# Kernel optimization log

Measured on AMD Instinct MI355X. Metric: run time of the kernel, lower is better.

## Reference

```python
import jax, jax.numpy as jnp
import numpy as np

EPS = 1e-6
N_HEADS = 6
N_POINTS = 4
B, LQ, C = 1, 96 * 96, 768


def _ln(x, w, b):
    mu = x.mean(-1, keepdims=True)
    var = ((x - mu) ** 2).mean(-1, keepdims=True)
    return (x - mu) * jax.lax.rsqrt(var + EPS) * w + b


def _corner(vbh, yi, xi, H, W):
    # vbh: [B, nH, H*W, Dh]; yi/xi: [B, nH, Lq, P] int32. Zero-padded OOB (grid_sample padding_mode='zeros').
    valid = (yi >= 0) & (yi < H) & (xi >= 0) & (xi < W)
    idx = jnp.clip(yi, 0, H - 1) * W + jnp.clip(xi, 0, W - 1)
    b, nh, lq, p = idx.shape
    g = jnp.take_along_axis(vbh, idx.reshape(b, nh, lq * p, 1), axis=2)
    g = g.reshape(b, nh, lq, p, vbh.shape[-1])
    return jnp.where(valid[..., None], g, jnp.zeros((), g.dtype))


def _msdeform(q, ref, feat, ss, so_w, so_b, aw_w, aw_b, vp_w, vp_b, op_w, op_b):
    # MSDeformAttn core: q [B,Lq,C], ref [B,Lq,L,2] in [0,1], feat [B,Len_in,C], ss np.int64 [L,2]=(H,W)
    b, lq, c = q.shape
    L = ss.shape[0]
    dh = c // N_HEADS
    value = (feat @ vp_w.T + vp_b).reshape(b, -1, N_HEADS, dh)
    offs = (q @ so_w.T + so_b).reshape(b, lq, N_HEADS, L, N_POINTS, 2)
    aw = jax.nn.softmax((q @ aw_w.T + aw_b).reshape(b, lq, N_HEADS, L * N_POINTS), -1)
    aw = aw.reshape(b, lq, N_HEADS, L, N_POINTS)
    # offset normalizer is (W, H) per level
    norm = jnp.asarray(np.ascontiguousarray(ss[:, ::-1]), dtype=q.dtype)  # [L,2]
    loc = ref[:, :, None, :, None, :] + offs / norm[None, None, None, :, None, :]
    out = jnp.zeros((b, N_HEADS, lq, dh), q.dtype)
    start = 0
    for l in range(L):
        H, W = int(ss[l, 0]), int(ss[l, 1])
        vbh = value[:, start:start + H * W].transpose(0, 2, 1, 3)  # [B,nH,H*W,Dh]
        # align_corners=False pixel coords: px = loc*W - 0.5
        px = loc[:, :, :, l, :, 0].transpose(0, 2, 1, 3) * W - 0.5  # [B,nH,Lq,P]
        py = loc[:, :, :, l, :, 1].transpose(0, 2, 1, 3) * H - 0.5
        x0 = jnp.floor(px).astype(jnp.int32)
        y0 = jnp.floor(py).astype(jnp.int32)
        fx = (px - x0)[..., None]
        fy = (py - y0)[..., None]
        samp = (_corner(vbh, y0, x0, H, W) * (1 - fy) * (1 - fx)
                + _corner(vbh, y0, x0 + 1, H, W) * (1 - fy) * fx
                + _corner(vbh, y0 + 1, x0, H, W) * fy * (1 - fx)
                + _corner(vbh, y0 + 1, x0 + 1, H, W) * fy * fx)  # [B,nH,Lq,P,Dh]
        w_l = aw[:, :, :, l, :].transpose(0, 2, 1, 3)[..., None]  # [B,nH,Lq,P,1]
        out = out + (samp * w_l).sum(3)
        start += H * W
    out = out.transpose(0, 2, 1, 3).reshape(b, lq, c)
    return out @ op_w.T + op_b


def setup_inputs() -> dict:
    key = jax.random.key(0)
    ks = jax.random.split(key, 14)
    lin = lambda k, o, i: 0.02 * jax.random.normal(k, (o, i), jnp.float32)
    return dict(
        query=jax.random.normal(ks[0], (B, LQ, C), jnp.float32),
        reference_points=jax.random.uniform(ks[1], (B, LQ, 1, 2), jnp.float32),
        feat=jax.random.normal(ks[2], (B, LQ, C), jnp.float32),
        feat_other_modalities=jax.random.normal(ks[3], (B, LQ, C), jnp.float32),
        spatial_shapes=np.array([[96, 96]], dtype=np.int64),
        level_start_index=np.array([0], dtype=np.int64),
        qn_w=jnp.ones(C), qn_b=jnp.zeros(C),
        fn_w=jnp.ones(C), fn_b=jnp.zeros(C),
        so_w=lin(ks[4], N_HEADS * N_POINTS * 2, C), so_b=0.02 * jax.random.normal(ks[12], (N_HEADS * N_POINTS * 2,), jnp.float32),
        aw_w=lin(ks[5], N_HEADS * N_POINTS, C), aw_b=jnp.zeros(N_HEADS * N_POINTS),
        vp_w=lin(ks[6], C, C), vp_b=jnp.zeros(C),
        op_w=lin(ks[7], C, C), op_b=jnp.zeros(C),
        gamma=0.02 * jax.random.normal(ks[8], (C,), jnp.float32),
        qn2_w=jnp.ones(C), qn2_b=jnp.zeros(C),
        fn2_w=jnp.ones(C), fn2_b=jnp.zeros(C),
        so2_w=lin(ks[9], N_HEADS * N_POINTS * 2, C), so2_b=0.02 * jax.random.normal(ks[13], (N_HEADS * N_POINTS * 2,), jnp.float32),
        aw2_w=lin(ks[10], N_HEADS * N_POINTS, C), aw2_b=jnp.zeros(N_HEADS * N_POINTS),
        vp2_w=lin(ks[11], C, C), vp2_b=jnp.zeros(C),
        op2_w=lin(jax.random.fold_in(key, 99), C, C), op2_b=jnp.zeros(C),
        gamma2=0.02 * jax.random.normal(jax.random.fold_in(key, 100), (C,), jnp.float32),
    )


def reference(query, reference_points, feat, feat_other_modalities, spatial_shapes, level_start_index,
              qn_w, qn_b, fn_w, fn_b, so_w, so_b, aw_w, aw_b, vp_w, vp_b, op_w, op_b, gamma,
              qn2_w, qn2_b, fn2_w, fn2_b, so2_w, so2_b, aw2_w, aw2_b, vp2_w, vp2_b, op2_w, op2_b, gamma2):
    ss = np.asarray(spatial_shapes)
    a = _msdeform(_ln(query, qn_w, qn_b), reference_points, _ln(feat, fn_w, fn_b), ss,
                  so_w, so_b, aw_w, aw_b, vp_w, vp_b, op_w, op_b)
    q = query + gamma * a
    a2 = _msdeform(_ln(q, qn2_w, qn2_b), reference_points,
                   _ln(feat_other_modalities, fn2_w, fn2_b), ss,
                   so2_w, so2_b, aw2_w, aw2_b, vp2_w, vp2_b, op2_w, op2_b)
    return q + gamma2 * a2
```

## Files before the change

kernel.cpp:

```cpp
#include <hip/hip_runtime.h>
#include <hip/hip_bf16.h>

typedef unsigned short u16;
typedef unsigned int u32;
typedef __attribute__((ext_vector_type(8))) short bf16x8;
typedef __attribute__((ext_vector_type(4))) float f32x4;
typedef __attribute__((ext_vector_type(4))) u32 u32x4;

#define LQ 9216
#define CC 768
#define NH 6
#define DH 128
#define HH 96
#define WW 96

__device__ __forceinline__ u16 f2bf(float f) {
  union { float f; u32 u; } x; x.f = f;
  u32 r = x.u + 0x7fff + ((x.u >> 16) & 1);
  return (u16)(r >> 16);
}
__device__ __forceinline__ float u2f(u32 u) {
  union { u32 u; float f; } x; x.u = u; return x.f;
}

__device__ __forceinline__ void gl_lds16(const void* g, void* l) {
  __builtin_amdgcn_global_load_lds((const __attribute__((address_space(1))) void*)g,
                                   (__attribute__((address_space(3))) void*)l, 16, 0, 0);
}

__global__ __launch_bounds__(256)
void prep_weights(const float* __restrict__ vp, const float* __restrict__ op,
                  const float* __restrict__ vp2, const float* __restrict__ op2,
                  const float* __restrict__ so, const float* __restrict__ aw,
                  const float* __restrict__ so2, const float* __restrict__ aw2,
                  const float* __restrict__ so_b, const float* __restrict__ aw_b,
                  const float* __restrict__ so2_b, const float* __restrict__ aw2_b,
                  u16* __restrict__ w4, u16* __restrict__ cat1, u16* __restrict__ cat2,
                  float* __restrict__ b1, float* __restrict__ b2) {
  const int i = blockIdx.x * 256 + threadIdx.x;
  const int NW = 589824;
  if (i < 4 * NW) {
    const int m = i / NW, r = i - m * NW;
    const float* s = (m == 0) ? vp : (m == 1) ? op : (m == 2) ? vp2 : op2;
    w4[i] = f2bf(s[r]);
  } else if (i < 4 * NW + 2 * 98304) {
    const int j = i - 4 * NW;
    const int which = j / 98304;
    const int r = j - which * 98304;
    const int row = r / 768, colr = r - row * 768;
    float v = 0.f;
    if (row < 48) v = (which ? so2 : so)[row * 768 + colr];
    else if (row < 72) v = (which ? aw2 : aw)[(row - 48) * 768 + colr];
    (which ? cat2 : cat1)[r] = f2bf(v);
  } else if (i < 4 * NW + 2 * 98304 + 256) {
    const int j = i - 4 * NW - 2 * 98304;
    const int which = j >> 7, row = j & 127;
    float v = 0.f;
    if (row < 48) v = (which ? so2_b : so_b)[row];
    else if (row < 72) v = (which ? aw2_b : aw_b)[row - 48];
    (which ? b2 : b1)[row] = v;
  }
}

__device__ __forceinline__ void ln_body(const float* __restrict__ x, const float* __restrict__ w,
                                        const float* __restrict__ b, u16* __restrict__ out, int row) {
  const int t = threadIdx.x;
  const float* xr = x + (size_t)row * CC;
  float v0 = xr[t], v1 = xr[t + 256], v2 = xr[t + 512];
  float s = v0 + v1 + v2;
  float ss = v0 * v0 + v1 * v1 + v2 * v2;
  #pragma unroll
  for (int o = 32; o > 0; o >>= 1) {
    s += __shfl_xor(s, o, 64);
    ss += __shfl_xor(ss, o, 64);
  }
  __shared__ float rs[4], rss[4];
  const int wv = t >> 6, ln = t & 63;
  if (ln == 0) { rs[wv] = s; rss[wv] = ss; }
  __syncthreads();
  s = rs[0] + rs[1] + rs[2] + rs[3];
  ss = rss[0] + rss[1] + rss[2] + rss[3];
  const float mu = s * (1.f / 768.f);
  const float var = ss * (1.f / 768.f) - mu * mu;
  const float rstd = rsqrtf(var + 1e-6f);
  u16* orow = out + (size_t)row * CC;
  orow[t]       = f2bf((v0 - mu) * rstd * w[t]       + b[t]);
  orow[t + 256] = f2bf((v1 - mu) * rstd * w[t + 256] + b[t + 256]);
  orow[t + 512] = f2bf((v2 - mu) * rstd * w[t + 512] + b[t + 512]);
}

__global__ __launch_bounds__(256)
void ln_to_bf16(const float* __restrict__ x, const float* __restrict__ w,
                const float* __restrict__ b, u16* __restrict__ out) {
  ln_body(x, w, b, out, blockIdx.x);
}

__global__ __launch_bounds__(256)
void ln3_to_bf16(const float* __restrict__ x0, const float* __restrict__ w0, const float* __restrict__ b0, u16* __restrict__ o0,
                 const float* __restrict__ x1, const float* __restrict__ w1, const float* __restrict__ b1, u16* __restrict__ o1,
                 const float* __restrict__ x2, const float* __restrict__ w2, const float* __restrict__ b2, u16* __restrict__ o2) {
  const int sel = blockIdx.y;
  const float* x = (sel == 0) ? x0 : (sel == 1) ? x1 : x2;
  const float* w = (sel == 0) ? w0 : (sel == 1) ? w1 : w2;
  const float* b = (sel == 0) ? b0 : (sel == 1) ? b1 : b2;
  u16* o = (sel == 0) ? o0 : (sel == 1) ? o1 : o2;
  ln_body(x, w, b, o, blockIdx.x);
}

template <int MODE>
__device__ __forceinline__ void gemm_core(const u16* __restrict__ A, const u16* __restrict__ W,
                                          const float* __restrict__ bias, void* __restrict__ outv,
                                          const float* __restrict__ res, const float* __restrict__ gamma,
                                          int M, int N, int K, int m0, int n0) {
  __shared__ u16 As[128 * 32];
  __shared__ u16 Bs[128 * 32];
  const int tid = threadIdx.x;
  const int wv = tid >> 6, lane = tid & 63;
  const int quad = lane >> 4, l16 = lane & 15;
  const int wm = wv & 1, wn = wv >> 1;
  const int srow = (wv << 4) + (lane >> 2);
  const int scol = (lane & 3) << 3;

  f32x4 acc[4][4];
  #pragma unroll
  for (int i = 0; i < 4; ++i)
    #pragma unroll
    for (int j = 0; j < 4; ++j)
      acc[i][j] = (f32x4){0.f, 0.f, 0.f, 0.f};

  const u16* ag = A + (size_t)(m0 + srow) * K + scol;
  const u16* bg = W + (size_t)(n0 + srow) * K + scol;
  u16* la = As + wv * 512 + lane * 8;
  u16* lb = Bs + wv * 512 + lane * 8;

  for (int k0 = 0; k0 < K; k0 += 32) {
    __syncthreads();
    gl_lds16(ag + k0, la);
    gl_lds16(ag + (size_t)64 * K + k0, la + 2048);
    gl_lds16(bg + k0, lb);
    gl_lds16(bg + (size_t)64 * K + k0, lb + 2048);
    __syncthreads();
    bf16x8 af[4], bfr[4];
    #pragma unroll
    for (int i = 0; i < 4; ++i)
      af[i] = *(const bf16x8*)(As + ((wm * 64 + i * 16 + l16) * 32 + quad * 8));
    #pragma unroll
    for (int j = 0; j < 4; ++j)
      bfr[j] = *(const bf16x8*)(Bs + ((wn * 64 + j * 16 + l16) * 32 + quad * 8));
    #pragma unroll
    for (int i = 0; i < 4; ++i)
      #pragma unroll
      for (int j = 0; j < 4; ++j)
        acc[i][j] = __builtin_amdgcn_mfma_f32_16x16x32_bf16(af[i], bfr[j], acc[i][j], 0, 0, 0);
  }

  #pragma unroll
  for (int i = 0; i < 4; ++i) {
    #pragma unroll
    for (int j = 0; j < 4; ++j) {
      const int col = n0 + wn * 64 + j * 16 + l16;
      const float bs = bias[col];
      #pragma unroll
      for (int r = 0; r < 4; ++r) {
        const int row = m0 + wm * 64 + i * 16 + quad * 4 + r;
        const float v = acc[i][j][r] + bs;
        const size_t o = (size_t)row * N + col;
        if (MODE == 0) ((u16*)outv)[o] = f2bf(v);
        else if (MODE == 1) ((float*)outv)[o] = v;
        else ((float*)outv)[o] = res[o] + gamma[col] * v;
      }
    }
  }
}

template <int MODE>
__global__ __launch_bounds__(256)
void gemm_bt(const u16* __restrict__ A, const u16* __restrict__ W,
             const float* __restrict__ bias, void* __restrict__ outv,
             const float* __restrict__ res, const float* __restrict__ gamma,
             int M, int N, int K) {
  gemm_core<MODE>(A, W, bias, outv, res, gamma, M, N, K, blockIdx.x * 128, blockIdx.y * 128);
}

__global__ __launch_bounds__(256)
void gemm_val_dual(const u16* __restrict__ A0, const u16* __restrict__ W0, const float* __restrict__ b0, u16* __restrict__ o0,
                   const u16* __restrict__ A1, const u16* __restrict__ W1, const float* __restrict__ b1, u16* __restrict__ o1,
                   int M, int N, int K) {
  const int z = blockIdx.z;
  const u16* A = z ? A1 : A0;
  const u16* W = z ? W1 : W0;
  const float* b = z ? b1 : b0;
  u16* o = z ? o1 : o0;
  gemm_core<0>(A, W, b, (void*)o, nullptr, nullptr, M, N, K, blockIdx.x * 128, blockIdx.y * 128);
}

__global__ __launch_bounds__(256)
void gemm_small(const u16* __restrict__ A, const u16* __restrict__ W,
                const float* __restrict__ bias, float* __restrict__ out,
                int M, int N, int K) {
  __shared__ u16 As[64 * 32];
  __shared__ u16 Bs[64 * 32];
  const int tid = threadIdx.x;
  const int wv = tid >> 6, lane = tid & 63;
  const int quad = lane >> 4, l16 = lane & 15;
  const int wm = wv & 1, wn = wv >> 1;
  const int m0 = blockIdx.x * 64, n0 = blockIdx.y * 64;
  const int srow = tid >> 2;
  const int scol = (tid & 3) << 3;

  f32x4 acc[2][2];
  #pragma unroll
  for (int i = 0; i < 2; ++i)
    #pragma unroll
    for (int j = 0; j < 2; ++j)
      acc[i][j] = (f32x4){0.f, 0.f, 0.f, 0.f};

  const u16* ag = A + (size_t)(m0 + srow) * K + scol;
  const u16* bg = W + (size_t)(n0 + srow) * K + scol;
  u16* la = As + tid * 8;
  u16* lb = Bs + tid * 8;

  for (int k0 = 0; k0 < K; k0 += 32) {
    __syncthreads();
    gl_lds16(ag + k0, la);
    gl_lds16(bg + k0, lb);
    __syncthreads();
    bf16x8 af[2], bfr[2];
    #pragma unroll
    for (int i = 0; i < 2; ++i)
      af[i] = *(const bf16x8*)(As + ((wm * 32 + i * 16 + l16) * 32 + quad * 8));
    #pragma unroll
    for (int j = 0; j < 2; ++j)
      bfr[j] = *(const bf16x8*)(Bs + ((wn * 32 + j * 16 + l16) * 32 + quad * 8));
    #pragma unroll
    for (int i = 0; i < 2; ++i)
      #pragma unroll
      for (int j = 0; j < 2; ++j)
        acc[i][j] = __builtin_amdgcn_mfma_f32_16x16x32_bf16(af[i], bfr[j], acc[i][j], 0, 0, 0);
  }

  #pragma unroll
  for (int i = 0; i < 2; ++i) {
    #pragma unroll
    for (int j = 0; j < 2; ++j) {
      const int col = n0 + wn * 32 + j * 16 + l16;
      const float bs = bias[col];
      #pragma unroll
      for (int r = 0; r < 4; ++r) {
        const int row = m0 + wm * 32 + i * 16 + quad * 4 + r;
        out[(size_t)row * N + col] = acc[i][j][r] + bs;
      }
    }
  }
}

__global__ __launch_bounds__(256)
void msds_sample(const u16* __restrict__ value, const float* __restrict__ offaw,
                 const float* __restrict__ ref, u16* __restrict__ out) {
  const int t = blockIdx.x * 256 + threadIdx.x;
  const int pi = t >> 4;
  const int gl = t & 15;
  const int q = pi / NH;
  const int h = pi - q * NH;
  const float* oa = offaw + (size_t)q * 128;
  const float rx = ref[q * 2] * (float)WW - 0.5f;
  const float ry = ref[q * 2 + 1] * (float)HH - 0.5f;

  const float lg0 = oa[48 + h * 4 + 0], lg1 = oa[48 + h * 4 + 1];
  const float lg2 = oa[48 + h * 4 + 2], lg3 = oa[48 + h * 4 + 3];
  const float mx = fmaxf(fmaxf(lg0, lg1), fmaxf(lg2, lg3));
  const float e0 = __expf(lg0 - mx), e1 = __expf(lg1 - mx);
  const float e2 = __expf(lg2 - mx), e3 = __expf(lg3 - mx);
  const float inv = 1.f / (e0 + e1 + e2 + e3);
  const float wp[4] = {e0 * inv, e1 * inv, e2 * inv, e3 * inv};

  float acc[8];
  #pragma unroll
  for (int k = 0; k < 8; ++k) acc[k] = 0.f;

  const u16* vbase = value + h * DH + gl * 8;
  #pragma unroll
  for (int p = 0; p < 4; ++p) {
    const float px = rx + oa[h * 8 + p * 2];
    const float py = ry + oa[h * 8 + p * 2 + 1];
    const float fxf = floorf(px), fyf = floorf(py);
    const int x0 = (int)fxf, y0 = (int)fyf;
    const float fx = px - fxf, fy = py - fyf;
    const float cw[4] = {wp[p] * (1.f - fy) * (1.f - fx), wp[p] * (1.f - fy) * fx,
                         wp[p] * fy * (1.f - fx),         wp[p] * fy * fx};
    #pragma unroll
    for (int c = 0; c < 4; ++c) {
      const int yy = y0 + (c >> 1);
      const int xx = x0 + (c & 1);
      const bool valid = (yy >= 0) & (yy < HH) & (xx >= 0) & (xx < WW);
      const int yc = min(max(yy, 0), HH - 1);
      const int xc = min(max(xx, 0), WW - 1);
      const float w2 = valid ? cw[c] : 0.f;
      const u32x4 u = *(const u32x4*)(vbase + (size_t)(yc * WW + xc) * CC);
      #pragma unroll
      for (int k = 0; k < 4; ++k) {
        acc[2 * k]     += w2 * u2f(u[k] << 16);
        acc[2 * k + 1] += w2 * u2f(u[k] & 0xffff0000u);
      }
    }
  }
  u32x4 o;
  #pragma unroll
  for (int k = 0; k < 4; ++k)
    o[k] = (u32)f2bf(acc[2 * k]) | ((u32)f2bf(acc[2 * k + 1]) << 16);
  *(u32x4*)(out + (size_t)q * CC + h * DH + gl * 8) = o;
}

extern "C" void kernel_launch(void* const* d_in, const int* in_sizes, int n_in,
                              void* d_out, int out_size, void* d_ws, size_t ws_size,
                              hipStream_t stream) {
  const float* query = (const float*)d_in[0];
  const float* refp  = (const float*)d_in[1];
  const float* feat  = (const float*)d_in[2];
  const float* feat2 = (const float*)d_in[3];
  const float* qn_w = (const float*)d_in[6];
  const float* qn_b = (const float*)d_in[7];
  const float* fn_w = (const float*)d_in[8];
  const float* fn_b = (const float*)d_in[9];
  const float* so_w = (const float*)d_in[10];
  const float* so_b = (const float*)d_in[11];
  const float* aw_w = (const float*)d_in[12];
  const float* aw_b = (const float*)d_in[13];
  const float* vp_w = (const float*)d_in[14];
  const float* vp_b = (const float*)d_in[15];
  const float* op_w = (const float*)d_in[16];
  const float* op_b = (const float*)d_in[17];
  const float* gamma = (const float*)d_in[18];
  const float* qn2_w = (const float*)d_in[19];
  const float* qn2_b = (const float*)d_in[20];
  const float* fn2_w = (const float*)d_in[21];
  const float* fn2_b = (const float*)d_in[22];
  const float* so2_w = (const float*)d_in[23];
  const float* so2_b = (const float*)d_in[24];
  const float* aw2_w = (const float*)d_in[25];
  const float* aw2_b = (const float*)d_in[26];
  const float* vp2_w = (const float*)d_in[27];
  const float* vp2_b = (const float*)d_in[28];
  const float* op2_w = (const float*)d_in[29];
  const float* op2_b = (const float*)d_in[30];
  const float* gamma2 = (const float*)d_in[31];

  char* ws = (char*)d_ws;
  size_t off = 0;
  auto alloc = [&](size_t bytes) -> void* {
    void* p = ws + off;
    off += (bytes + 255) & ~(size_t)255;
    return p;
  };
  u16* w4    = (u16*)alloc((size_t)4 * 589824 * 2);
  u16* cat1  = (u16*)alloc((size_t)98304 * 2);
  u16* cat2  = (u16*)alloc((size_t)98304 * 2);
  float* b1  = (float*)alloc(128 * 4);
  float* b2  = (float*)alloc(128 * 4);
  u16* qn    = (u16*)alloc((size_t)LQ * CC * 2);
  u16* fn    = (u16*)alloc((size_t)LQ * CC * 2);
  u16* fn2   = (u16*)alloc((size_t)LQ * CC * 2);
  u16* val1  = (u16*)alloc((size_t)LQ * CC * 2);
  u16* val2  = (u16*)alloc((size_t)LQ * CC * 2);
  float* offaw = (float*)alloc((size_t)LQ * 128 * 4);
  float* qbuf  = (float*)alloc((size_t)LQ * CC * 4);

  dim3 blk(256);
  dim3 gbig(LQ / 128, CC / 128), gdual(LQ / 128, CC / 128, 2), gsm(LQ / 64, 2);

  prep_weights<<<9985, blk, 0, stream>>>(vp_w, op_w, vp2_w, op2_w, so_w, aw_w, so2_w, aw2_w,
                                         so_b, aw_b, so2_b, aw2_b, w4, cat1, cat2, b1, b2);
  ln3_to_bf16<<<dim3(LQ, 3), blk, 0, stream>>>(query, qn_w, qn_b, qn,
                                               feat, fn_w, fn_b, fn,
                                               feat2, fn2_w, fn2_b, fn2);
  gemm_val_dual<<<gdual, blk, 0, stream>>>(fn, w4, vp_b, val1,
                                           fn2, w4 + 2 * 589824, vp2_b, val2, LQ, CC, CC);
  gemm_small<<<gsm, blk, 0, stream>>>(qn, cat1, b1, offaw, LQ, 128, CC);
  msds_sample<<<LQ * NH / 16, blk, 0, stream>>>(val1, offaw, refp, fn);
  gemm_bt<2><<<gbig, blk, 0, stream>>>(fn, w4 + 589824, op_b, (void*)qbuf, query, gamma, LQ, CC, CC);
  ln_to_bf16<<<LQ, blk, 0, stream>>>(qbuf, qn2_w, qn2_b, qn);
  gemm_small<<<gsm, blk, 0, stream>>>(qn, cat2, b2, offaw, LQ, 128, CC);
  msds_sample<<<LQ * NH / 16, blk, 0, stream>>>(val2, offaw, refp, fn2);
  gemm_bt<2><<<gbig, blk, 0, stream>>>(fn2, w4 + 3 * 589824, op2_b, d_out, qbuf, gamma2, LQ, CC, CC);
}
```

Before: 361.3 us.

## Retile GEMMs to 128x64 tiles with K=64 steps and unify small GEMM

The shared GEMM core is templated on M-tile size. Big GEMMs now use 128x64 output tiles instead of 128x128, and every GEMM stages K=64 per iteration, which halves the barrier count and doubles the MFMAs between barriers. Launch bounds now request 5 blocks per CU, trading per-block accumulator registers and reuse for more resident blocks and a doubled grid. The separate small GEMM kernel is replaced by the templated core with TM=64.

```diff
diff --git a/kernel.cpp b/kernel.cpp
--- a/kernel.cpp
+++ b/kernel.cpp
@@ -107,62 +107,72 @@
   ln_body(x, w, b, o, blockIdx.x);
 }
 
-template <int MODE>
+template <int TM, int MODE>
 __device__ __forceinline__ void gemm_core(const u16* __restrict__ A, const u16* __restrict__ W,
                                           const float* __restrict__ bias, void* __restrict__ outv,
                                           const float* __restrict__ res, const float* __restrict__ gamma,
-                                          int M, int N, int K, int m0, int n0) {
-  __shared__ u16 As[128 * 32];
-  __shared__ u16 Bs[128 * 32];
+                                          int N, int K, int m0, int n0) {
+  constexpr int FI = TM / 32;
+  constexpr int NIA = TM / 32;
+  __shared__ u16 As[TM * 64];
+  __shared__ u16 Bs[64 * 64];
   const int tid = threadIdx.x;
   const int wv = tid >> 6, lane = tid & 63;
   const int quad = lane >> 4, l16 = lane & 15;
   const int wm = wv & 1, wn = wv >> 1;
-  const int srow = (wv << 4) + (lane >> 2);
-  const int scol = (lane & 3) << 3;
-
-  f32x4 acc[4][4];
-  #pragma unroll
-  for (int i = 0; i < 4; ++i)
-    #pragma unroll
-    for (int j = 0; j < 4; ++j)
+  const int sr4 = lane >> 2;
+  const int sc = (lane & 3) << 3;
+
+  f32x4 acc[FI][2];
+  #pragma unroll
+  for (int i = 0; i < FI; ++i)
+    #pragma unroll
+    for (int j = 0; j < 2; ++j)
       acc[i][j] = (f32x4){0.f, 0.f, 0.f, 0.f};
 
-  const u16* ag = A + (size_t)(m0 + srow) * K + scol;
-  const u16* bg = W + (size_t)(n0 + srow) * K + scol;
-  u16* la = As + wv * 512 + lane * 8;
-  u16* lb = Bs + wv * 512 + lane * 8;
-
-  for (int k0 = 0; k0 < K; k0 += 32) {
+  for (int k0 = 0; k0 < K; k0 += 64) {
     __syncthreads();
-    gl_lds16(ag + k0, la);
-    gl_lds16(ag + (size_t)64 * K + k0, la + 2048);
-    gl_lds16(bg + k0, lb);
-    gl_lds16(bg + (size_t)64 * K + k0, lb + 2048);
+    #pragma unroll
+    for (int j = 0; j < NIA; ++j) {
+      const int g = wv * NIA + j;
+      const int p = g & 1, rb = g >> 1;
+      gl_lds16(A + (size_t)(m0 + rb * 16 + sr4) * K + (k0 + p * 32 + sc),
+               (char*)As + p * (TM * 64) + rb * 1024 + lane * 16);
+    }
+    #pragma unroll
+    for (int j = 0; j < 2; ++j) {
+      const int g = wv * 2 + j;
+      const int p = g & 1, rb = g >> 1;
+      gl_lds16(W + (size_t)(n0 + rb * 16 + sr4) * K + (k0 + p * 32 + sc),
+               (char*)Bs + p * 4096 + rb * 1024 + lane * 16);
+    }
     __syncthreads();
-    bf16x8 af[4], bfr[4];
-    #pragma unroll
-    for (int i = 0; i < 4; ++i)
-      af[i] = *(const bf16x8*)(As + ((wm * 64 + i * 16 + l16) * 32 + quad * 8));
-    #pragma unroll
-    for (int j = 0; j < 4; ++j)
-      bfr[j] = *(const bf16x8*)(Bs + ((wn * 64 + j * 16 + l16) * 32 + quad * 8));
-    #pragma unroll
-    for (int i = 0; i < 4; ++i)
-      #pragma unroll
-      for (int j = 0; j < 4; ++j)
-        acc[i][j] = __builtin_amdgcn_mfma_f32_16x16x32_bf16(af[i], bfr[j], acc[i][j], 0, 0, 0);
-  }
-
-  #pragma unroll
-  for (int i = 0; i < 4; ++i) {
-    #pragma unroll
-    for (int j = 0; j < 4; ++j) {
-      const int col = n0 + wn * 64 + j * 16 + l16;
+    #pragma unroll
+    for (int kk = 0; kk < 2; ++kk) {
+      bf16x8 af[FI], bfr[2];
+      #pragma unroll
+      for (int i = 0; i < FI; ++i)
+        af[i] = *(const bf16x8*)(As + kk * (TM * 32) + (wm * (TM / 2) + i * 16 + l16) * 32 + quad * 8);
+      #pragma unroll
+      for (int j = 0; j < 2; ++j)
+        bfr[j] = *(const bf16x8*)(Bs + kk * 2048 + (wn * 32 + j * 16 + l16) * 32 + quad * 8);
+      #pragma unroll
+      for (int i = 0; i < FI; ++i)
+        #pragma unroll
+        for (int j = 0; j < 2; ++j)
+          acc[i][j] = __builtin_amdgcn_mfma_f32_16x16x32_bf16(af[i], bfr[j], acc[i][j], 0, 0, 0);
+    }
+  }
+
+  #pragma unroll
+  for (int i = 0; i < FI; ++i) {
+    #pragma unroll
+    for (int j = 0; j < 2; ++j) {
+      const int col = n0 + wn * 32 + j * 16 + l16;
       const float bs = bias[col];
       #pragma unroll
       for (int r = 0; r < 4; ++r) {
-        const int row = m0 + wm * 64 + i * 16 + quad * 4 + r;
+        const int row = m0 + wm * (TM / 2) + i * 16 + quad * 4 + r;
         const float v = acc[i][j][r] + bs;
         const size_t o = (size_t)row * N + col;
         if (MODE == 0) ((u16*)outv)[o] = f2bf(v);
@@ -174,84 +184,31 @@
 }
 
 template <int MODE>
-__global__ __launch_bounds__(256)
+__global__ __launch_bounds__(256, 5)
 void gemm_bt(const u16* __restrict__ A, const u16* __restrict__ W,
              const float* __restrict__ bias, void* __restrict__ outv,
              const float* __restrict__ res, const float* __restrict__ gamma,
-             int M, int N, int K) {
-  gemm_core<MODE>(A, W, bias, outv, res, gamma, M, N, K, blockIdx.x * 128, blockIdx.y * 128);
-}
-
-__global__ __launch_bounds__(256)
+             int N, int K) {
+  gemm_core<128, MODE>(A, W, bias, outv, res, gamma, N, K, blockIdx.x * 128, blockIdx.y * 64);
+}
+
+__global__ __launch_bounds__(256, 5)
 void gemm_val_dual(const u16* __restrict__ A0, const u16* __restrict__ W0, const float* __restrict__ b0, u16* __restrict__ o0,
                    const u16* __restrict__ A1, const u16* __restrict__ W1, const float* __restrict__ b1, u16* __restrict__ o1,
-                   int M, int N, int K) {
+                   int N, int K) {
   const int z = blockIdx.z;
   const u16* A = z ? A1 : A0;
   const u16* W = z ? W1 : W0;
   const float* b = z ? b1 : b0;
   u16* o = z ? o1 : o0;
-  gemm_core<0>(A, W, b, (void*)o, nullptr, nullptr, M, N, K, blockIdx.x * 128, blockIdx.y * 128);
-}
-
-__global__ __launch_bounds__(256)
+  gemm_core<128, 0>(A, W, b, (void*)o, nullptr, nullptr, N, K, blockIdx.x * 128, blockIdx.y * 64);
+}
+
+__global__ __launch_bounds__(256, 5)
 void gemm_small(const u16* __restrict__ A, const u16* __restrict__ W,
                 const float* __restrict__ bias, float* __restrict__ out,
-                int M, int N, int K) {
-  __shared__ u16 As[64 * 32];
-  __shared__ u16 Bs[64 * 32];
-  const int tid = threadIdx.x;
-  const int wv = tid >> 6, lane = tid & 63;
-  const int quad = lane >> 4, l16 = lane & 15;
-  const int wm = wv & 1, wn = wv >> 1;
-  const int m0 = blockIdx.x * 64, n0 = blockIdx.y * 64;
-  const int srow = tid >> 2;
-  const int scol = (tid & 3) << 3;
-
-  f32x4 acc[2][2];
-  #pragma unroll
-  for (int i = 0; i < 2; ++i)
-    #pragma unroll
-    for (int j = 0; j < 2; ++j)
-      acc[i][j] = (f32x4){0.f, 0.f, 0.f, 0.f};
-
-  const u16* ag = A + (size_t)(m0 + srow) * K + scol;
-  const u16* bg = W + (size_t)(n0 + srow) * K + scol;
-  u16* la = As + tid * 8;
-  u16* lb = Bs + tid * 8;
-
-  for (int k0 = 0; k0 < K; k0 += 32) {
-    __syncthreads();
-    gl_lds16(ag + k0, la);
-    gl_lds16(bg + k0, lb);
-    __syncthreads();
-    bf16x8 af[2], bfr[2];
-    #pragma unroll
-    for (int i = 0; i < 2; ++i)
-      af[i] = *(const bf16x8*)(As + ((wm * 32 + i * 16 + l16) * 32 + quad * 8));
-    #pragma unroll
-    for (int j = 0; j < 2; ++j)
-      bfr[j] = *(const bf16x8*)(Bs + ((wn * 32 + j * 16 + l16) * 32 + quad * 8));
-    #pragma unroll
-    for (int i = 0; i < 2; ++i)
-      #pragma unroll
-      for (int j = 0; j < 2; ++j)
-        acc[i][j] = __builtin_amdgcn_mfma_f32_16x16x32_bf16(af[i], bfr[j], acc[i][j], 0, 0, 0);
-  }
-
-  #pragma unroll
-  for (int i = 0; i < 2; ++i) {
-    #pragma unroll
-    for (int j = 0; j < 2; ++j) {
-      const int col = n0 + wn * 32 + j * 16 + l16;
-      const float bs = bias[col];
-      #pragma unroll
-      for (int r = 0; r < 4; ++r) {
-        const int row = m0 + wm * 32 + i * 16 + quad * 4 + r;
-        out[(size_t)row * N + col] = acc[i][j][r] + bs;
-      }
-    }
-  }
+                int N, int K) {
+  gemm_core<64, 1>(A, W, bias, (void*)out, nullptr, nullptr, N, K, blockIdx.x * 64, blockIdx.y * 64);
 }
 
 __global__ __launch_bounds__(256)
@@ -366,7 +323,7 @@
   float* qbuf  = (float*)alloc((size_t)LQ * CC * 4);
 
   dim3 blk(256);
-  dim3 gbig(LQ / 128, CC / 128), gdual(LQ / 128, CC / 128, 2), gsm(LQ / 64, 2);
+  dim3 gbig(LQ / 128, CC / 64), gdual(LQ / 128, CC / 64, 2), gsm(LQ / 64, 2);
 
   prep_weights<<<9985, blk, 0, stream>>>(vp_w, op_w, vp2_w, op2_w, so_w, aw_w, so2_w, aw2_w,
                                          so_b, aw_b, so2_b, aw2_b, w4, cat1, cat2, b1, b2);
@@ -374,12 +331,12 @@
                                                feat, fn_w, fn_b, fn,
                                                feat2, fn2_w, fn2_b, fn2);
   gemm_val_dual<<<gdual, blk, 0, stream>>>(fn, w4, vp_b, val1,
-                                           fn2, w4 + 2 * 589824, vp2_b, val2, LQ, CC, CC);
-  gemm_small<<<gsm, blk, 0, stream>>>(qn, cat1, b1, offaw, LQ, 128, CC);
+                                           fn2, w4 + 2 * 589824, vp2_b, val2, CC, CC);
+  gemm_small<<<gsm, blk, 0, stream>>>(qn, cat1, b1, offaw, 128, CC);
   msds_sample<<<LQ * NH / 16, blk, 0, stream>>>(val1, offaw, refp, fn);
-  gemm_bt<2><<<gbig, blk, 0, stream>>>(fn, w4 + 589824, op_b, (void*)qbuf, query, gamma, LQ, CC, CC);
+  gemm_bt<2><<<gbig, blk, 0, stream>>>(fn, w4 + 589824, op_b, (void*)qbuf, query, gamma, CC, CC);
   ln_to_bf16<<<LQ, blk, 0, stream>>>(qbuf, qn2_w, qn2_b, qn);
-  gemm_small<<<gsm, blk, 0, stream>>>(qn, cat2, b2, offaw, LQ, 128, CC);
+  gemm_small<<<gsm, blk, 0, stream>>>(qn, cat2, b2, offaw, 128, CC);
   msds_sample<<<LQ * NH / 16, blk, 0, stream>>>(val2, offaw, refp, fn2);
-  gemm_bt<2><<<gbig, blk, 0, stream>>>(fn2, w4 + 3 * 589824, op2_b, d_out, qbuf, gamma2, LQ, CC, CC);
-}
+  gemm_bt<2><<<gbig, blk, 0, stream>>>(fn2, w4 + 3 * 589824, op2_b, d_out, qbuf, gamma2, CC, CC);
+}
```

After: 342.0 us. -5.3%, faster.
